# Performance work log

Hardware: AMD Instinct MI355X
Metric: run time of the kernel (lower is better)

## Reference

```python
import math
import jax, jax.numpy as jnp
import numpy as np

B, T = 64, 8192
D_OUT = 128
KPOS = 2
DT = 1.0 / 240.0


def _ema(x, alpha):
    # x: [B, T] -> causal EMA along T: acc = alpha*acc + (1-alpha)*x_t, acc0 = 0
    def step(acc, xt):
        acc = alpha * acc + (1.0 - alpha) * xt
        return acc, acc
    _, ys = jax.lax.scan(step, jnp.zeros(x.shape[0], x.dtype), x.T)  # ys: [T, B]
    return ys.T


def _fourier_axis(coord, logw, phi):
    # coord: [B,T]; logw, phi: [K] -> [B,T,2K]
    w = jnp.exp(logw)[None, None, :]
    arg = 2.0 * math.pi * coord[..., None] * w + phi[None, None, :]
    return jnp.concatenate([jnp.sin(arg), jnp.cos(arg)], axis=-1)


def setup_inputs() -> dict:
    key = jax.random.key(0)
    ks = jax.random.split(key, 4)
    gaze_xy = jax.random.normal(ks[0], (B, T, 2), dtype=jnp.float32) * 5.0
    D_in = 4 * KPOS + 12  # 20
    # xavier-uniform style init for the two Linear layers
    lim1 = math.sqrt(6.0 / (D_in + D_OUT))
    lim2 = math.sqrt(6.0 / (D_OUT + D_OUT))
    W1 = jax.random.uniform(ks[1], (D_in, D_OUT), jnp.float32, -lim1, lim1)
    b1 = jnp.zeros((D_OUT,), jnp.float32)
    W2 = jax.random.uniform(ks[2], (D_OUT, D_OUT), jnp.float32, -lim2, lim2)
    b2 = jnp.zeros((D_OUT,), jnp.float32)
    return {
        "gaze_xy": gaze_xy,
        "pos_logw_x": jnp.full((KPOS,), math.log(1.0 / 64.0), jnp.float32),
        "pos_phi_x": jnp.zeros((KPOS,), jnp.float32),
        "pos_logw_y": jnp.full((KPOS,), math.log(1.0 / 64.0), jnp.float32),
        "pos_phi_y": jnp.zeros((KPOS,), jnp.float32),
        "sac_log_thr": jnp.asarray(math.log(200.0), jnp.float32),
        "sac_invT": jnp.asarray(0.05, jnp.float32),
        "W1": W1, "b1": b1, "W2": W2, "b2": b2,
    }


def reference(gaze_xy, pos_logw_x, pos_phi_x, pos_logw_y, pos_phi_y,
              sac_log_thr, sac_invT, W1, b1, W2, b2):
    dt = max(DT, 1e-6)
    eps = 1e-6
    # causal diff with first-frame prepend (diff at t=0 is zero)
    prev = jnp.concatenate([gaze_xy[:, :1], gaze_xy[:, :-1]], axis=1)
    v = (gaze_xy - prev) / dt                      # [B,T,2]
    v_prev = jnp.concatenate([v[:, :1], v[:, :-1]], axis=1)
    a = (v - v_prev) / dt                          # [B,T,2]
    speed = jnp.linalg.norm(v, axis=-1)            # [B,T]
    inv_sp = 1.0 / (speed + eps)
    dir_cos = v[..., 0] * inv_sp
    dir_sin = v[..., 1] * inv_sp
    a_par = (v * a).sum(-1) * inv_sp
    a_perp = (v[..., 0] * a[..., 1] - v[..., 1] * a[..., 0]) * inv_sp
    thr = jnp.exp(sac_log_thr)
    gate = jax.nn.sigmoid(sac_invT * (speed - thr))  # [B,T]
    q_fast = _ema(gate, 0.8)
    q_slow = _ema(gate, 0.95)
    scalars = jnp.stack([v[..., 0], v[..., 1], speed, dir_cos, dir_sin,
                         a[..., 0], a[..., 1], a_par, a_perp,
                         gate, q_fast, q_slow], axis=-1)  # [B,T,12]
    fx = _fourier_axis(gaze_xy[..., 0], pos_logw_x, pos_phi_x)  # [B,T,4]
    fy = _fourier_axis(gaze_xy[..., 1], pos_logw_y, pos_phi_y)  # [B,T,4]
    feats = jnp.concatenate([fx, fy, scalars], axis=-1)         # [B,T,20]
    h = jax.nn.gelu(feats @ W1 + b1, approximate=False)
    h = jax.nn.gelu(h @ W2 + b2, approximate=False)
    return h
```

## Files before the change

kernel.cpp:

```cpp
#include <hip/hip_runtime.h>
#include <math.h>

#define BB 64
#define TT 8192
#define NTILES 8192
#define MLP_GRID 2048
#define EMA_GRID 512

typedef short short8 __attribute__((ext_vector_type(8)));
typedef float f32x4 __attribute__((ext_vector_type(4)));

__device__ __forceinline__ unsigned short f2bf(float x) {
    unsigned int u = __float_as_uint(x);
    u += 0x7fffu + ((u >> 16) & 1u);
    return (unsigned short)(u >> 16);
}

__device__ __forceinline__ unsigned int f2bf2(float lo, float hi) {
    return (unsigned int)f2bf(lo) | ((unsigned int)f2bf(hi) << 16);
}

__device__ __forceinline__ float fast_sigmoid(float z) {
    return __builtin_amdgcn_rcpf(1.0f + __expf(-z));
}

__device__ __forceinline__ float fast_gelu(float x) {
    return x * fast_sigmoid(1.702f * x);
}

__global__ __launch_bounds__(256) void ema_kernel(
    const float* __restrict__ gaze, const float* __restrict__ logthr,
    const float* __restrict__ invT, float* __restrict__ qf, float* __restrict__ qs)
{
    __shared__ __align__(16) float sg[1280];
    const int tid = threadIdx.x;
    const int b   = blockIdx.x >> 3;
    const int t0  = (blockIdx.x & 7) << 10;
    const float thr = __expf(logthr[0]);
    const float sT  = invT[0];
    const float2* gz = (const float2*)gaze + (size_t)b * TT;

    #pragma unroll
    for (int it = 0; it < 5; ++it) {
        int i = tid + it * 256;
        int t = t0 - 252 + i;
        float val = 0.0f;
        if (t >= 0 && t < TT) {
            float vx = 0.0f, vy = 0.0f;
            if (t > 0) {
                float2 a = gz[t], p = gz[t - 1];
                vx = (a.x - p.x) * 240.0f;
                vy = (a.y - p.y) * 240.0f;
            }
            float speed = sqrtf(vx * vx + vy * vy);
            val = 1.0f / (1.0f + __expf(-sT * (speed - thr)));
        }
        sg[i] = val;
    }
    __syncthreads();

    const float4* sg4 = (const float4*)sg;
    float Sf = 0.0f, Ss = 0.0f;
    float wf = 0.16f;
    float ws = 0.0475f;
    for (int u = 62; u >= 0; --u) {
        float4 qv = sg4[tid + u];
        float hf = fmaf(0.8f,  fmaf(0.8f,  fmaf(0.8f,  qv.x, qv.y), qv.z), qv.w);
        Sf = fmaf(wf, hf, Sf);  wf *= 0.4096f;
        float hs = fmaf(0.95f, fmaf(0.95f, fmaf(0.95f, qv.x, qv.y), qv.z), qv.w);
        Ss = fmaf(ws, hs, Ss);  ws *= 0.81450625f;
    }
    float4 r = sg4[tid + 63];
    float g0v = r.x, g1v = r.y, g2v = r.z, g3v = r.w;

    float o0 = Sf + 0.2f * g0v;
    float o1 = fmaf(0.8f,   Sf, 0.2f * fmaf(0.8f, g0v, g1v));
    float o2 = fmaf(0.64f,  Sf, 0.2f * (g2v + 0.8f * g1v + 0.64f * g0v));
    float o3 = fmaf(0.512f, Sf, 0.2f * (g3v + 0.8f * g2v + 0.64f * g1v + 0.512f * g0v));

    float p0 = Ss + 0.05f * g0v;
    float p1 = fmaf(0.95f,     Ss, 0.05f * fmaf(0.95f, g0v, g1v));
    float p2 = fmaf(0.9025f,   Ss, 0.05f * (g2v + 0.95f * g1v + 0.9025f * g0v));
    float p3 = fmaf(0.857375f, Ss, 0.05f * (g3v + 0.95f * g2v + 0.9025f * g1v + 0.857375f * g0v));

    const size_t ob = (size_t)b * TT + t0 + 4 * tid;
    *(float4*)(qf + ob) = make_float4(o0, o1, o2, o3);
    *(float4*)(qs + ob) = make_float4(p0, p1, p2, p3);
}

__global__ __launch_bounds__(256, 4) void mlp_kernel(
    const float* __restrict__ gaze,
    const float* __restrict__ lwx, const float* __restrict__ phx,
    const float* __restrict__ lwy, const float* __restrict__ phy,
    const float* __restrict__ logthr, const float* __restrict__ invT,
    const float* __restrict__ W1, const float* __restrict__ b1,
    const float* __restrict__ W2, const float* __restrict__ b2,
    const float* __restrict__ qf, const float* __restrict__ qs,
    float* __restrict__ out)
{
    __shared__ __align__(16) unsigned short sW2[128 * 136];
    __shared__ __align__(16) float sb2[128];

    const int tid  = threadIdx.x;
    const int lane = tid & 63;
    const int wave = tid >> 6;
    const int c    = lane & 15;
    const int q    = lane >> 4;

    #pragma unroll
    for (int it = 0; it < 32; ++it) {
        int i  = tid + it * 256;
        int n  = i & 127;
        int kp = i >> 7;
        unsigned short lo = f2bf(W2[(2 * kp) * 128 + n]);
        unsigned short hi = f2bf(W2[(2 * kp + 1) * 128 + n]);
        *(unsigned int*)&sW2[n * 136 + 2 * kp] = ((unsigned int)hi << 16) | lo;
    }
    if (tid < 128) sb2[tid] = b2[tid];

    short8 B1[8];
    #pragma unroll
    for (int j = 0; j < 8; ++j) {
        const int ch = 32 * (j & 3) + 8 * (c >> 2) + 4 * (j >> 2) + (c & 3);
        union { unsigned short u[8]; short8 v; } tmp;
        #pragma unroll
        for (int u = 0; u < 8; ++u) {
            int k = 8 * q + u;
            float w = 0.0f;
            if (k < 20)       w = W1[k * 128 + ch];
            else if (k == 20) w = b1[ch];
            tmp.u[u] = (k <= 20) ? f2bf(w) : (unsigned short)0;
        }
        B1[j] = tmp.v;
    }

    const float twopi = 6.283185307179586f;
    const float cwx0 = twopi * __expf(lwx[0]), cwx1 = twopi * __expf(lwx[1]);
    const float cwy0 = twopi * __expf(lwy[0]), cwy1 = twopi * __expf(lwy[1]);
    const float px0 = phx[0], px1 = phx[1], py0 = phy[0], py1 = phy[1];
    const float thr = __expf(logthr[0]), sT = invT[0];

    __syncthreads();

    const float2* gz = (const float2*)gaze;

    for (int tile = blockIdx.x; tile < NTILES; tile += MLP_GRID) {
        const int b   = tile >> 7;
        const int t0  = (tile & 127) << 6;
        const int t   = t0 + wave * 16 + c;
        const int idx = b * TT + t;

        float2 g0 = gz[idx];
        float2 g1 = (t > 0) ? gz[idx - 1] : g0;
        float2 g2 = (t > 1) ? gz[idx - 2] : g1;
        float vx = (g0.x - g1.x) * 240.0f;
        float vy = (g0.y - g1.y) * 240.0f;
        float vpx = (g1.x - g2.x) * 240.0f;
        float vpy = (g1.y - g2.y) * 240.0f;
        float ax = (vx - vpx) * 240.0f;
        float ay = (vy - vpy) * 240.0f;
        float speed  = sqrtf(vx * vx + vy * vy);
        float inv_sp = __builtin_amdgcn_rcpf(speed + 1e-6f);

        float f[8] = {0.f, 0.f, 0.f, 0.f, 0.f, 0.f, 0.f, 0.f};
        if (q == 0) {
            __sincosf(fmaf(g0.x, cwx0, px0), &f[0], &f[2]);
            __sincosf(fmaf(g0.x, cwx1, px1), &f[1], &f[3]);
            __sincosf(fmaf(g0.y, cwy0, py0), &f[4], &f[6]);
            __sincosf(fmaf(g0.y, cwy1, py1), &f[5], &f[7]);
        } else if (q == 1) {
            f[0] = vx; f[1] = vy; f[2] = speed;
            f[3] = vx * inv_sp; f[4] = vy * inv_sp;
            f[5] = ax; f[6] = ay;
            f[7] = (vx * ax + vy * ay) * inv_sp;
        } else if (q == 2) {
            f[0] = (vx * ay - vy * ax) * inv_sp;
            f[1] = fast_sigmoid(sT * (speed - thr));
            f[2] = qf[idx];
            f[3] = qs[idx];
            f[4] = 1.0f;
        }

        union { unsigned short u[8]; short8 v; } A1;
        #pragma unroll
        for (int k = 0; k < 8; ++k) A1.u[k] = f2bf(f[k]);

        f32x4 acc1[8];
        #pragma unroll
        for (int j = 0; j < 8; ++j) {
            f32x4 z = {0.f, 0.f, 0.f, 0.f};
            acc1[j] = __builtin_amdgcn_mfma_f32_16x16x32_bf16(B1[j], A1.v, z, 0, 0, 0);
        }

        short8 A2[4];
        #pragma unroll
        for (int s = 0; s < 4; ++s) {
            union { unsigned int w[4]; short8 v; } t2;
            t2.w[0] = f2bf2(fast_gelu(acc1[s][0]),     fast_gelu(acc1[s][1]));
            t2.w[1] = f2bf2(fast_gelu(acc1[s][2]),     fast_gelu(acc1[s][3]));
            t2.w[2] = f2bf2(fast_gelu(acc1[s + 4][0]), fast_gelu(acc1[s + 4][1]));
            t2.w[3] = f2bf2(fast_gelu(acc1[s + 4][2]), fast_gelu(acc1[s + 4][3]));
            A2[s] = t2.v;
        }

        float* ob = out + (size_t)(b * TT + t0 + wave * 16 + c) * 128 + 4 * q;
        #pragma unroll
        for (int j = 0; j < 8; ++j) {
            f32x4 acc = *(const f32x4*)&sb2[16 * j + 4 * q];
            #pragma unroll
            for (int s = 0; s < 4; ++s) {
                short8 W2f = *(const short8*)&sW2[(16 * j + c) * 136 + 32 * s + 8 * q];
                acc = __builtin_amdgcn_mfma_f32_16x16x32_bf16(W2f, A2[s], acc, 0, 0, 0);
            }
            f32x4 o;
            #pragma unroll
            for (int r = 0; r < 4; ++r) o[r] = fast_gelu(acc[r]);
            *(f32x4*)(ob + 16 * j) = o;
        }
    }
}

extern "C" void kernel_launch(void* const* d_in, const int* in_sizes, int n_in,
                              void* d_out, int out_size, void* d_ws, size_t ws_size,
                              hipStream_t stream)
{
    const float* gaze   = (const float*)d_in[0];
    const float* lwx    = (const float*)d_in[1];
    const float* phx    = (const float*)d_in[2];
    const float* lwy    = (const float*)d_in[3];
    const float* phy    = (const float*)d_in[4];
    const float* logthr = (const float*)d_in[5];
    const float* invT   = (const float*)d_in[6];
    const float* W1     = (const float*)d_in[7];
    const float* b1     = (const float*)d_in[8];
    const float* W2     = (const float*)d_in[9];
    const float* b2     = (const float*)d_in[10];
    float* out = (float*)d_out;

    float* qf = (float*)d_ws;
    float* qs = qf + BB * TT;

    ema_kernel<<<EMA_GRID, 256, 0, stream>>>(gaze, logthr, invT, qf, qs);
    mlp_kernel<<<MLP_GRID, 256, 0, stream>>>(gaze, lwx, phx, lwy, phy, logthr, invT,
                                             W1, b1, W2, b2, qf, qs, out);
}
```

Baseline: 310.8 us.

## Software-pipeline MLP tiles: overlap next tile's front half with current back half

Replaces the grid-stride tile loop with a fully unrolled four-tile schedule. The feature and first-layer stage of the next tile is computed before the second-layer stage and store of the previous one, so loads and transcendental work can overlap with MFMA and store work. The per-quadrant feature branches become branchless selects that compute every feature on every lane, and launch bounds drop from 4 to 3 blocks per SM to allow more registers. The cost is extra redundant ALU work and lower occupancy. The code also hardcodes that NTILES equals four times MLP_GRID.

Result: slower. 470.7 us (+51.5%).

```diff
diff --git a/kernel.cpp b/kernel.cpp
--- a/kernel.cpp
+++ b/kernel.cpp
@@ -88,7 +88,102 @@
     *(float4*)(qs + ob) = make_float4(p0, p1, p2, p3);
 }
 
-__global__ __launch_bounds__(256, 4) void mlp_kernel(
+struct Frags { short8 a[4]; };
+struct B1s   { short8 b[8]; };
+
+__device__ __forceinline__ Frags mlp_front(
+    int tile, int wave, int c, int q,
+    const float2* __restrict__ gz, const float* __restrict__ qf,
+    const float* __restrict__ qs, const B1s& B1,
+    float cwx0, float cwx1, float cwy0, float cwy1,
+    float px0, float px1, float py0, float py1,
+    float thr, float sT)
+{
+    const int b   = tile >> 7;
+    const int t0  = (tile & 127) << 6;
+    const int t   = t0 + wave * 16 + c;
+    const int idx = b * TT + t;
+
+    float2 g0 = gz[idx];
+    float2 g1 = (t > 0) ? gz[idx - 1] : g0;
+    float2 g2 = (t > 1) ? gz[idx - 2] : g1;
+    float qfv = qf[idx];
+    float qsv = qs[idx];
+
+    float vx = (g0.x - g1.x) * 240.0f;
+    float vy = (g0.y - g1.y) * 240.0f;
+    float vpx = (g1.x - g2.x) * 240.0f;
+    float vpy = (g1.y - g2.y) * 240.0f;
+    float ax = (vx - vpx) * 240.0f;
+    float ay = (vy - vpy) * 240.0f;
+    float speed  = sqrtf(vx * vx + vy * vy);
+    float inv_sp = __builtin_amdgcn_rcpf(speed + 1e-6f);
+
+    float s0, c0s, s1, c1s, s2, c2s, s3, c3s;
+    __sincosf(fmaf(g0.x, cwx0, px0), &s0, &c0s);
+    __sincosf(fmaf(g0.x, cwx1, px1), &s1, &c1s);
+    __sincosf(fmaf(g0.y, cwy0, py0), &s2, &c2s);
+    __sincosf(fmaf(g0.y, cwy1, py1), &s3, &c3s);
+    float gate = fast_sigmoid(sT * (speed - thr));
+
+    const bool q0 = (q == 0), q1 = (q == 1), q2 = (q == 2);
+    float f[8];
+    f[0] = q0 ? s0  : (q1 ? vx            : (q2 ? (vx * ay - vy * ax) * inv_sp : 0.f));
+    f[1] = q0 ? s1  : (q1 ? vy            : (q2 ? gate : 0.f));
+    f[2] = q0 ? c0s : (q1 ? speed         : (q2 ? qfv  : 0.f));
+    f[3] = q0 ? c1s : (q1 ? vx * inv_sp   : (q2 ? qsv  : 0.f));
+    f[4] = q0 ? s2  : (q1 ? vy * inv_sp   : (q2 ? 1.0f : 0.f));
+    f[5] = q0 ? s3  : (q1 ? ax            : 0.f);
+    f[6] = q0 ? c2s : (q1 ? ay            : 0.f);
+    f[7] = q0 ? c3s : (q1 ? (vx * ax + vy * ay) * inv_sp : 0.f);
+
+    union { unsigned short u[8]; short8 v; } A1;
+    #pragma unroll
+    for (int k = 0; k < 8; ++k) A1.u[k] = f2bf(f[k]);
+
+    f32x4 acc1[8];
+    #pragma unroll
+    for (int j = 0; j < 8; ++j) {
+        f32x4 z = {0.f, 0.f, 0.f, 0.f};
+        acc1[j] = __builtin_amdgcn_mfma_f32_16x16x32_bf16(B1.b[j], A1.v, z, 0, 0, 0);
+    }
+
+    Frags r;
+    #pragma unroll
+    for (int s = 0; s < 4; ++s) {
+        union { unsigned int w[4]; short8 v; } t2;
+        t2.w[0] = f2bf2(fast_gelu(acc1[s][0]),     fast_gelu(acc1[s][1]));
+        t2.w[1] = f2bf2(fast_gelu(acc1[s][2]),     fast_gelu(acc1[s][3]));
+        t2.w[2] = f2bf2(fast_gelu(acc1[s + 4][0]), fast_gelu(acc1[s + 4][1]));
+        t2.w[3] = f2bf2(fast_gelu(acc1[s + 4][2]), fast_gelu(acc1[s + 4][3]));
+        r.a[s] = t2.v;
+    }
+    return r;
+}
+
+__device__ __forceinline__ void mlp_back(
+    int tile, int wave, int c, int q, const Frags& A2,
+    const unsigned short* sW2p, const float* sb2p, float* __restrict__ out)
+{
+    const int b  = tile >> 7;
+    const int t0 = (tile & 127) << 6;
+    float* ob = out + (size_t)(b * TT + t0 + wave * 16 + c) * 128 + 4 * q;
+    #pragma unroll
+    for (int j = 0; j < 8; ++j) {
+        f32x4 acc = *(const f32x4*)&sb2p[16 * j + 4 * q];
+        #pragma unroll
+        for (int s = 0; s < 4; ++s) {
+            short8 W2f = *(const short8*)&sW2p[(16 * j + c) * 136 + 32 * s + 8 * q];
+            acc = __builtin_amdgcn_mfma_f32_16x16x32_bf16(W2f, A2.a[s], acc, 0, 0, 0);
+        }
+        f32x4 o;
+        #pragma unroll
+        for (int r = 0; r < 4; ++r) o[r] = fast_gelu(acc[r]);
+        *(f32x4*)(ob + 16 * j) = o;
+    }
+}
+
+__global__ __launch_bounds__(256, 3) void mlp_kernel(
     const float* __restrict__ gaze,
     const float* __restrict__ lwx, const float* __restrict__ phx,
     const float* __restrict__ lwy, const float* __restrict__ phy,
@@ -118,7 +213,7 @@
     }
     if (tid < 128) sb2[tid] = b2[tid];
 
-    short8 B1[8];
+    B1s B1;
     #pragma unroll
     for (int j = 0; j < 8; ++j) {
         const int ch = 32 * (j & 3) + 8 * (c >> 2) + 4 * (j >> 2) + (c & 3);
@@ -131,7 +226,7 @@
             else if (k == 20) w = b1[ch];
             tmp.u[u] = (k <= 20) ? f2bf(w) : (unsigned short)0;
         }
-        B1[j] = tmp.v;
+        B1.b[j] = tmp.v;
     }
 
     const float twopi = 6.283185307179586f;
@@ -143,81 +238,20 @@
     __syncthreads();
 
     const float2* gz = (const float2*)gaze;
-
-    for (int tile = blockIdx.x; tile < NTILES; tile += MLP_GRID) {
-        const int b   = tile >> 7;
-        const int t0  = (tile & 127) << 6;
-        const int t   = t0 + wave * 16 + c;
-        const int idx = b * TT + t;
-
-        float2 g0 = gz[idx];
-        float2 g1 = (t > 0) ? gz[idx - 1] : g0;
-        float2 g2 = (t > 1) ? gz[idx - 2] : g1;
-        float vx = (g0.x - g1.x) * 240.0f;
-        float vy = (g0.y - g1.y) * 240.0f;
-        float vpx = (g1.x - g2.x) * 240.0f;
-        float vpy = (g1.y - g2.y) * 240.0f;
-        float ax = (vx - vpx) * 240.0f;
-        float ay = (vy - vpy) * 240.0f;
-        float speed  = sqrtf(vx * vx + vy * vy);
-        float inv_sp = __builtin_amdgcn_rcpf(speed + 1e-6f);
-
-        float f[8] = {0.f, 0.f, 0.f, 0.f, 0.f, 0.f, 0.f, 0.f};
-        if (q == 0) {
-            __sincosf(fmaf(g0.x, cwx0, px0), &f[0], &f[2]);
-            __sincosf(fmaf(g0.x, cwx1, px1), &f[1], &f[3]);
-            __sincosf(fmaf(g0.y, cwy0, py0), &f[4], &f[6]);
-            __sincosf(fmaf(g0.y, cwy1, py1), &f[5], &f[7]);
-        } else if (q == 1) {
-            f[0] = vx; f[1] = vy; f[2] = speed;
-            f[3] = vx * inv_sp; f[4] = vy * inv_sp;
-            f[5] = ax; f[6] = ay;
-            f[7] = (vx * ax + vy * ay) * inv_sp;
-        } else if (q == 2) {
-            f[0] = (vx * ay - vy * ax) * inv_sp;
-            f[1] = fast_sigmoid(sT * (speed - thr));
-            f[2] = qf[idx];
-            f[3] = qs[idx];
-            f[4] = 1.0f;
-        }
-
-        union { unsigned short u[8]; short8 v; } A1;
-        #pragma unroll
-        for (int k = 0; k < 8; ++k) A1.u[k] = f2bf(f[k]);
-
-        f32x4 acc1[8];
-        #pragma unroll
-        for (int j = 0; j < 8; ++j) {
-            f32x4 z = {0.f, 0.f, 0.f, 0.f};
-            acc1[j] = __builtin_amdgcn_mfma_f32_16x16x32_bf16(B1[j], A1.v, z, 0, 0, 0);
-        }
-
-        short8 A2[4];
-        #pragma unroll
-        for (int s = 0; s < 4; ++s) {
-            union { unsigned int w[4]; short8 v; } t2;
-            t2.w[0] = f2bf2(fast_gelu(acc1[s][0]),     fast_gelu(acc1[s][1]));
-            t2.w[1] = f2bf2(fast_gelu(acc1[s][2]),     fast_gelu(acc1[s][3]));
-            t2.w[2] = f2bf2(fast_gelu(acc1[s + 4][0]), fast_gelu(acc1[s + 4][1]));
-            t2.w[3] = f2bf2(fast_gelu(acc1[s + 4][2]), fast_gelu(acc1[s + 4][3]));
-            A2[s] = t2.v;
-        }
-
-        float* ob = out + (size_t)(b * TT + t0 + wave * 16 + c) * 128 + 4 * q;
-        #pragma unroll
-        for (int j = 0; j < 8; ++j) {
-            f32x4 acc = *(const f32x4*)&sb2[16 * j + 4 * q];
-            #pragma unroll
-            for (int s = 0; s < 4; ++s) {
-                short8 W2f = *(const short8*)&sW2[(16 * j + c) * 136 + 32 * s + 8 * q];
-                acc = __builtin_amdgcn_mfma_f32_16x16x32_bf16(W2f, A2[s], acc, 0, 0, 0);
-            }
-            f32x4 o;
-            #pragma unroll
-            for (int r = 0; r < 4; ++r) o[r] = fast_gelu(acc[r]);
-            *(f32x4*)(ob + 16 * j) = o;
-        }
-    }
+    const int base = blockIdx.x;
+
+    Frags f0 = mlp_front(base,                wave, c, q, gz, qf, qs, B1,
+                         cwx0, cwx1, cwy0, cwy1, px0, px1, py0, py1, thr, sT);
+    Frags f1 = mlp_front(base +     MLP_GRID, wave, c, q, gz, qf, qs, B1,
+                         cwx0, cwx1, cwy0, cwy1, px0, px1, py0, py1, thr, sT);
+    mlp_back(base,                wave, c, q, f0, sW2, sb2, out);
+    Frags f2 = mlp_front(base + 2 * MLP_GRID, wave, c, q, gz, qf, qs, B1,
+                         cwx0, cwx1, cwy0, cwy1, px0, px1, py0, py1, thr, sT);
+    mlp_back(base +     MLP_GRID, wave, c, q, f1, sW2, sb2, out);
+    Frags f3 = mlp_front(base + 3 * MLP_GRID, wave, c, q, gz, qf, qs, B1,
+                         cwx0, cwx1, cwy0, cwy1, px0, px1, py0, py1, thr, sT);
+    mlp_back(base + 2 * MLP_GRID, wave, c, q, f2, sW2, sb2, out);
+    mlp_back(base + 3 * MLP_GRID, wave, c, q, f3, sW2, sb2, out);
 }
 
 extern "C" void kernel_launch(void* const* d_in, const int* in_sizes, int n_in,
```
